# Performance work log

Hardware: AMD Instinct MI355X
Metric: run time of the kernel (lower is better)

Reference implementation:

```python
import jax, jax.numpy as jnp
import numpy as np

B, S, D, MD = 4, 4096, 1024, 512
SCALE = 0.02  # init scale for weights


def _layernorm(x, g, b, eps=1e-5):
    m = jnp.mean(x, axis=-1, keepdims=True)
    v = jnp.mean((x - m) ** 2, axis=-1, keepdims=True)
    return (x - m) * jax.lax.rsqrt(v + eps) * g + b


def _mem_mlp(h, W0, W1):
    # MemoryMLP depth=2: linear -> gelu -> linear (no biases)
    return jax.nn.gelu(h @ W0) @ W1


def _assoc_scan(gates, inputs):
    # state_t = g_t * state_{t-1} + in_t, over the seq axis (axis=1)
    def step(state, gi):
        g, i = gi
        s = g * state + i
        return s, s
    init = jnp.zeros_like(inputs[:, 0])
    _, out = jax.lax.scan(step, init, (jnp.moveaxis(gates, 1, 0), jnp.moveaxis(inputs, 1, 0)))
    return jnp.moveaxis(out, 1, 0)


def setup_inputs() -> dict:
    key = jax.random.key(0)
    ks = jax.random.split(key, 10)
    return {
        "x": jax.random.normal(ks[0], (B, S, D), jnp.float32),
        "Wd": jax.random.normal(ks[1], (D, MD), jnp.float32) * SCALE,
        "bd": jnp.zeros((MD,), jnp.float32),
        "Wu": jax.random.normal(ks[2], (MD, D), jnp.float32) * SCALE,
        "bu": jnp.zeros((D,), jnp.float32),
        "Wq": jax.random.normal(ks[3], (MD, MD), jnp.float32) * SCALE,
        "bq": jnp.zeros((MD,), jnp.float32),
        "Wk": jax.random.normal(ks[4], (MD, MD), jnp.float32) * SCALE,
        "bk": jnp.zeros((MD,), jnp.float32),
        "Wv": jax.random.normal(ks[5], (MD, MD), jnp.float32) * SCALE,
        "bv": jnp.zeros((MD,), jnp.float32),
        "q_gamma": jnp.ones((MD,), jnp.float32),
        "q_beta": jnp.zeros((MD,), jnp.float32),
        "k_gamma": jnp.ones((MD,), jnp.float32),
        "k_beta": jnp.zeros((MD,), jnp.float32),
        "W0": jax.random.normal(ks[6], (MD, MD), jnp.float32) * SCALE,
        "W1": jax.random.normal(ks[7], (MD, MD), jnp.float32) * SCALE,
        "adaptive_lr": jnp.full((1,), 0.01, jnp.float32),
        "forget_factor": jnp.full((1,), 0.1, jnp.float32),
    }


def reference(x, Wd, bd, Wu, bu, Wq, bq, Wk, bk, Wv, bv,
              q_gamma, q_beta, k_gamma, k_beta, W0, W1,
              adaptive_lr, forget_factor):
    h = x @ Wd + bd                                   # [B,S,MD] down_proj
    q = _layernorm(h @ Wq + bq, q_gamma, q_beta)      # q_norm(to_queries)
    k = _layernorm(h @ Wk + bk, k_gamma, k_beta)      # k_norm(to_keys)
    v = h @ Wv + bv                                   # to_values
    retrieved = _mem_mlp(q, W0, W1)                   # memory read
    pred = _mem_mlp(k, W0, W1)                        # memory store pred
    # per-token surprise: MSE over feature dim
    surprise = jnp.mean((pred - v) ** 2, axis=-1, keepdims=True)  # [B,S,1]
    gate_val = 1.0 - jax.nn.sigmoid(forget_factor)[0]
    gates = jnp.full((B, S, 1), 1.0, jnp.float32) * gate_val
    inputs = adaptive_lr[0] * surprise * v            # surprise-weighted write
    scanned = _assoc_scan(gates, inputs)              # sequential recurrence
    out = (retrieved + scanned) @ Wu + bu             # up_proj
    return out
```

## Files before the change

kernel.cpp:

```cpp
#include <hip/hip_runtime.h>
#include <hip/hip_bf16.h>
#include <math.h>

#define B_    4
#define S_    4096
#define DD    1024
#define MD    512
#define NTOK  16384
#define CHUNK 32
#define NCH   128

typedef unsigned short u16;
typedef unsigned int u32;
typedef __attribute__((ext_vector_type(8))) short short8;
typedef __attribute__((ext_vector_type(4))) float f32x4;
typedef __attribute__((ext_vector_type(4))) unsigned short us4;

__device__ __forceinline__ float bf2f(u16 u) {
    u32 x = ((u32)u) << 16;
    return __builtin_bit_cast(float, x);
}
__device__ __forceinline__ u16 f2bf(float f) {
    u32 x = __builtin_bit_cast(u32, f);
    u32 lsb = (x >> 16) & 1u;
    x += 0x7fffu + lsb;
    return (u16)(x >> 16);
}
__device__ __forceinline__ float gelu_f(float x) {
    float x3 = x * x * x;
    return 0.5f * x * (1.0f + tanhf(0.7978845608028654f * (x + 0.044715f * x3)));
}
__device__ __forceinline__ float gate_from_ff(const float* ff) {
    return 1.0f - 1.0f / (1.0f + expf(-ff[0]));
}

#define GLDS(gp, lp) __builtin_amdgcn_global_load_lds( \
    (const __attribute__((address_space(1))) void*)(gp), \
    (__attribute__((address_space(3))) void*)(lp), 16, 0, 0)

template<int EPI, int HB, int OUTBF>
__global__ __launch_bounds__(512) void gemm_bf16_k(
    const u16* __restrict__ A0, const u16* __restrict__ A1, const u16* __restrict__ A2,
    const u16* __restrict__ W0p, const u16* __restrict__ W1p, const u16* __restrict__ W2p,
    const float* __restrict__ c0, const float* __restrict__ c1, const float* __restrict__ c2,
    void* __restrict__ o0, void* __restrict__ o1, void* __restrict__ o2,
    int K, int OM)
{
    __shared__ __align__(16) u16 Al[3][256 * 32];
    __shared__ __align__(16) u16 Bl[3][128 * 32];
    const int tid = threadIdx.x;
    const int w = tid >> 6, l = tid & 63;

    const int z = blockIdx.z;
    const u16* A      = (z == 0) ? A0 : (z == 1) ? A1 : A2;
    const u16* BT     = (z == 0) ? W0p : (z == 1) ? W1p : W2p;
    const float* bias = (z == 0) ? c0 : (z == 1) ? c1 : c2;
    void* outp        = (z == 0) ? o0 : (z == 1) ? o1 : o2;

    const int rowBase = blockIdx.y * 256, colBase = blockIdx.x * 128;
    const int wm = (w >> 1) * 64, wn = (w & 1) * 64;
    const int lr = l & 15;

    float bj[4] = {0.f, 0.f, 0.f, 0.f};
    if (HB) {
#pragma unroll
        for (int n = 0; n < 4; ++n) bj[n] = bias[colBase + wn + n * 16 + lr];
        asm volatile("" :: "v"(bj[0]), "v"(bj[1]), "v"(bj[2]), "v"(bj[3]));
    }
    asm volatile("s_waitcnt vmcnt(0)" ::: "memory");
    __builtin_amdgcn_sched_barrier(0);

    const int srow = l >> 2;
    const int skoff = ((l & 3) ^ (srow & 3)) * 8;
    const u16* Ag0 = A  + (size_t)(rowBase + (2 * w) * 16 + srow) * K + skoff;
    const u16* Ag1 = A  + (size_t)(rowBase + (2 * w + 1) * 16 + srow) * K + skoff;
    const u16* Bg0 = BT + (size_t)(colBase + w * 16 + srow) * K + skoff;

    f32x4 acc[4][4];
#pragma unroll
    for (int i = 0; i < 4; ++i)
#pragma unroll
        for (int j = 0; j < 4; ++j) acc[i][j] = (f32x4){0.f, 0.f, 0.f, 0.f};

    const int KT = K >> 5;

#define STAGE(kt, buf) do { \
    const size_t ko = (size_t)(kt) << 5; \
    GLDS(Ag0 + ko, &Al[buf][((2 * w) * 16) * 32]); \
    GLDS(Ag1 + ko, &Al[buf][((2 * w + 1) * 16) * 32]); \
    GLDS(Bg0 + ko, &Bl[buf][(w * 16) * 32]); \
} while (0)

    STAGE(0, 0);
    STAGE(1, 1);
    asm volatile("s_waitcnt vmcnt(3)" ::: "memory");
    __builtin_amdgcn_sched_barrier(0);
    __builtin_amdgcn_s_barrier();
    __builtin_amdgcn_sched_barrier(0);

    const int rsw = (((l >> 4) ^ (l & 3)) << 3);
    int bt = 0;
    for (int t = 0; t < KT; ++t) {
        int bs = bt + 2; if (bs >= 3) bs -= 3;
        const bool more = (t + 2) < KT;
        if (more) STAGE(t + 2, bs);
        short8 af[4], bfr[4];
#pragma unroll
        for (int m = 0; m < 4; ++m)
            af[m] = *(const short8*)&Al[bt][(wm + m * 16 + lr) * 32 + rsw];
#pragma unroll
        for (int n = 0; n < 4; ++n)
            bfr[n] = *(const short8*)&Bl[bt][(wn + n * 16 + lr) * 32 + rsw];
#pragma unroll
        for (int m = 0; m < 4; ++m)
#pragma unroll
            for (int n = 0; n < 4; ++n)
                acc[m][n] = __builtin_amdgcn_mfma_f32_16x16x32_bf16(af[m], bfr[n], acc[m][n], 0, 0, 0);
        if (more) { asm volatile("s_waitcnt vmcnt(3)" ::: "memory"); }
        else      { asm volatile("s_waitcnt vmcnt(0)" ::: "memory"); }
        __builtin_amdgcn_sched_barrier(0);
        __builtin_amdgcn_s_barrier();
        __builtin_amdgcn_sched_barrier(0);
        bt = (bt + 1 == 3) ? 0 : bt + 1;
    }
#undef STAGE

    const int g4 = (l >> 4) * 4;
    const int col0 = colBase + wn;

    if (OUTBF) {
        u16* scr = &Al[0][0] + w * 1024;
        u16* ob = (u16*)outp;
        const bool odd = l & 1;
        const int lrp = lr & ~1;
#pragma unroll
        for (int m = 0; m < 4; ++m) {
            const int baseRow = rowBase + wm + m * 16;
            float vq[4][4];
#pragma unroll
            for (int n = 0; n < 4; ++n) {
#pragma unroll
                for (int q = 0; q < 4; ++q) {
                    float vv = acc[m][n][q] + bj[n];
                    if (EPI == 1) vv = gelu_f(vv);
                    vq[n][q] = vv;
                }
            }
#pragma unroll
            for (int n = 0; n < 4; ++n) {
                float pv[4];
#pragma unroll
                for (int q = 0; q < 4; ++q) pv[q] = __shfl_xor(vq[n][q], 1);
                const int q0 = odd ? 2 : 0;
#pragma unroll
                for (int j = 0; j < 2; ++j) {
                    const int qq = q0 + j;
                    float lo = odd ? pv[qq] : vq[n][qq];
                    float hi = odd ? vq[n][qq] : pv[qq];
                    u32 word = (u32)f2bf(lo) | ((u32)f2bf(hi) << 16);
                    *(u32*)&scr[(g4 + qq) * 64 + n * 16 + lrp] = word;
                }
            }
            asm volatile("s_waitcnt lgkmcnt(0)" ::: "memory");
            __builtin_amdgcn_sched_barrier(0);
            short8 r0 = *(const short8*)&scr[(l >> 3) * 64 + (l & 7) * 8];
            short8 r1 = *(const short8*)&scr[((l >> 3) + 8) * 64 + (l & 7) * 8];
            const size_t gaddr = (size_t)(baseRow + (l >> 3)) * OM + col0 + (l & 7) * 8;
            *(short8*)(ob + gaddr) = r0;
            *(short8*)(ob + gaddr + (size_t)8 * OM) = r1;
            __builtin_amdgcn_sched_barrier(0);
        }
    } else {
#pragma unroll
        for (int n = 0; n < 4; ++n) {
            const int col = col0 + n * 16 + lr;
#pragma unroll
            for (int m = 0; m < 4; ++m) {
                const int row0 = rowBase + wm + m * 16 + g4;
#pragma unroll
                for (int q = 0; q < 4; ++q) {
                    float vv = acc[m][n][q] + bj[n];
                    if (EPI == 1) vv = gelu_f(vv);
                    ((float*)outp)[(size_t)(row0 + q) * OM + col] = vv;
                }
            }
        }
    }
}

__global__ __launch_bounds__(256) void cvt_bf16_k(const float* __restrict__ in,
                                                  u16* __restrict__ out, int n)
{
    size_t i = ((size_t)blockIdx.x * 256 + threadIdx.x) * 8;
    if (i + 8 > (size_t)n) return;
    float4 a = *(const float4*)(in + i);
    float4 b = *(const float4*)(in + i + 4);
    short8 o;
    o[0] = (short)f2bf(a.x); o[1] = (short)f2bf(a.y);
    o[2] = (short)f2bf(a.z); o[3] = (short)f2bf(a.w);
    o[4] = (short)f2bf(b.x); o[5] = (short)f2bf(b.y);
    o[6] = (short)f2bf(b.z); o[7] = (short)f2bf(b.w);
    *(short8*)(out + i) = o;
}

__global__ __launch_bounds__(256) void wtrans_k(const float* __restrict__ W,
                                                u16* __restrict__ WT, int K, int M)
{
    __shared__ float t[32][33];
    const int tx = threadIdx.x, ty = threadIdx.y;
    const int m0 = blockIdx.x * 32, k0 = blockIdx.y * 32;
#pragma unroll
    for (int i = 0; i < 4; ++i)
        t[ty + i * 8][tx] = W[(size_t)(k0 + ty + i * 8) * M + m0 + tx];
    __syncthreads();
#pragma unroll
    for (int i = 0; i < 4; ++i)
        WT[(size_t)(m0 + ty + i * 8) * K + k0 + tx] = f2bf(t[tx][ty + i * 8]);
}

__global__ __launch_bounds__(256) void wtrans5_k(
    const float* __restrict__ Wa, const float* __restrict__ Wb,
    const float* __restrict__ Wc, const float* __restrict__ Wd_,
    const float* __restrict__ We,
    u16* __restrict__ Ta, u16* __restrict__ Tb, u16* __restrict__ Tc,
    u16* __restrict__ Td, u16* __restrict__ Te)
{
    __shared__ float t[32][33];
    const float* W; u16* T;
    switch (blockIdx.z) {
        case 0: W = Wa; T = Ta; break;
        case 1: W = Wb; T = Tb; break;
        case 2: W = Wc; T = Tc; break;
        case 3: W = Wd_; T = Td; break;
        default: W = We; T = Te; break;
    }
    const int tx = threadIdx.x, ty = threadIdx.y;
    const int m0 = blockIdx.x * 32, k0 = blockIdx.y * 32;
#pragma unroll
    for (int i = 0; i < 4; ++i)
        t[ty + i * 8][tx] = W[(size_t)(k0 + ty + i * 8) * 512 + m0 + tx];
    __syncthreads();
#pragma unroll
    for (int i = 0; i < 4; ++i)
        T[(size_t)(m0 + ty + i * 8) * 512 + k0 + tx] = f2bf(t[tx][ty + i * 8]);
}

__global__ __launch_bounds__(256) void ln2_k(u16* __restrict__ X0, u16* __restrict__ X1,
                                             const float* __restrict__ g0, const float* __restrict__ b0,
                                             const float* __restrict__ g1, const float* __restrict__ b1)
{
    const int row = blockIdx.x, tid = threadIdx.x;
    u16* x = (blockIdx.y ? X1 : X0) + (size_t)row * MD;
    const float* g = blockIdx.y ? g1 : g0;
    const float* b = blockIdx.y ? b1 : b0;
    float v0 = bf2f(x[tid]), v1 = bf2f(x[tid + 256]);
    float s = v0 + v1, q = v0 * v0 + v1 * v1;
#pragma unroll
    for (int off = 32; off > 0; off >>= 1) {
        s += __shfl_down(s, off);
        q += __shfl_down(q, off);
    }
    __shared__ float redS[4], redQ[4];
    __shared__ float s_mean, s_rstd;
    const int lane = tid & 63, w = tid >> 6;
    if (lane == 0) { redS[w] = s; redQ[w] = q; }
    __syncthreads();
    if (tid == 0) {
        float S = redS[0] + redS[1] + redS[2] + redS[3];
        float Q = redQ[0] + redQ[1] + redQ[2] + redQ[3];
        float m = S * (1.f / 512.f);
        float var = Q * (1.f / 512.f) - m * m;
        s_mean = m; s_rstd = rsqrtf(var + 1e-5f);
    }
    __syncthreads();
    const float m = s_mean, rs = s_rstd;
    x[tid]       = f2bf((v0 - m) * rs * g[tid]       + b[tid]);
    x[tid + 256] = f2bf((v1 - m) * rs * g[tid + 256] + b[tid + 256]);
}

__global__ __launch_bounds__(256) void surprise_k(const u16* __restrict__ pred,
                                                  const u16* __restrict__ v,
                                                  const float* __restrict__ lr_p,
                                                  float* __restrict__ coef)
{
    const int row = blockIdx.x, tid = threadIdx.x;
    const u16* pp = pred + (size_t)row * MD;
    const u16* vp = v + (size_t)row * MD;
    float d0 = bf2f(pp[tid]) - bf2f(vp[tid]);
    float d1 = bf2f(pp[tid + 256]) - bf2f(vp[tid + 256]);
    float q = d0 * d0 + d1 * d1;
#pragma unroll
    for (int off = 32; off > 0; off >>= 1) q += __shfl_down(q, off);
    __shared__ float redQ[4];
    const int lane = tid & 63, w = tid >> 6;
    if (lane == 0) redQ[w] = q;
    __syncthreads();
    if (tid == 0) {
        float Q = redQ[0] + redQ[1] + redQ[2] + redQ[3];
        coef[row] = lr_p[0] * (Q * (1.f / 512.f));
    }
}

__global__ __launch_bounds__(256) void scan1_k(u16* __restrict__ io,
                                               const float* __restrict__ coef,
                                               const float* __restrict__ ff,
                                               float* __restrict__ carry)
{
    const int idx = blockIdx.x * blockDim.x + threadIdx.x;
    const int d4 = (idx & 127) * 4;
    const int c = (idx >> 7) & (NCH - 1);
    const int b = idx >> 14;
    const float g = gate_from_ff(ff);
    const int tok0 = b * S_ + c * CHUNK;
    u16* p = io + (size_t)tok0 * MD + d4;
    const float* cf = coef + tok0;
    float s0 = 0.f, s1 = 0.f, s2 = 0.f, s3 = 0.f;
#pragma unroll 4
    for (int t = 0; t < CHUNK; ++t) {
        us4 vv = *(const us4*)(p + (size_t)t * MD);
        const float ct = cf[t];
        s0 = fmaf(g, s0, ct * bf2f(vv.x));
        s1 = fmaf(g, s1, ct * bf2f(vv.y));
        s2 = fmaf(g, s2, ct * bf2f(vv.z));
        s3 = fmaf(g, s3, ct * bf2f(vv.w));
        us4 ov = { f2bf(s0), f2bf(s1), f2bf(s2), f2bf(s3) };
        *(us4*)(p + (size_t)t * MD) = ov;
    }
    float4 cw = { s0, s1, s2, s3 };
    *(float4*)(carry + ((size_t)b * NCH + c) * MD + d4) = cw;
}

__global__ __launch_bounds__(256) void scan2_k(const float* __restrict__ carry,
                                               const float* __restrict__ ff,
                                               float* __restrict__ Sin)
{
    const int idx = blockIdx.x * blockDim.x + threadIdx.x;
    const int d = idx & (MD - 1);
    const int b = idx >> 9;
    const float g = gate_from_ff(ff);
    const float gL = powf(g, (float)CHUNK);
    float p = 0.f;
    for (int c = 0; c < NCH; ++c) {
        Sin[((size_t)b * NCH + c) * MD + d] = p;
        p = carry[((size_t)b * NCH + c) * MD + d] + gL * p;
    }
}

__global__ __launch_bounds__(256) void scan3_k(const u16* __restrict__ loc,
                                               const float* __restrict__ Sin,
                                               const u16* __restrict__ retr,
                                               const float* __restrict__ ff,
                                               u16* __restrict__ fin)
{
    const size_t idx = (size_t)blockIdx.x * blockDim.x + threadIdx.x;
    const int d4 = (int)(idx & 127) * 4;
    const int t = (int)((idx >> 7) & (S_ - 1));
    const int b = (int)(idx >> 19);
    const int c = t >> 5, tl = t & (CHUNK - 1);
    const float g = gate_from_ff(ff);
    const float f = exp2f((float)(tl + 1) * log2f(g));
    const size_t row = (size_t)(b * S_ + t) * MD + d4;
    us4 lv = *(const us4*)(loc + row);
    us4 rv = *(const us4*)(retr + row);
    float4 sv = *(const float4*)(Sin + ((size_t)b * NCH + c) * MD + d4);
    us4 ov;
    ov.x = f2bf(bf2f(lv.x) + f * sv.x + bf2f(rv.x));
    ov.y = f2bf(bf2f(lv.y) + f * sv.y + bf2f(rv.y));
    ov.z = f2bf(bf2f(lv.z) + f * sv.z + bf2f(rv.z));
    ov.w = f2bf(bf2f(lv.w) + f * sv.w + bf2f(rv.w));
    *(us4*)(fin + row) = ov;
}

extern "C" void kernel_launch(void* const* d_in, const int* in_sizes, int n_in,
                              void* d_out, int out_size, void* d_ws, size_t ws_size,
                              hipStream_t stream) {
    const float* x   = (const float*)d_in[0];
    const float* Wd  = (const float*)d_in[1];
    const float* bd  = (const float*)d_in[2];
    const float* Wu  = (const float*)d_in[3];
    const float* bu  = (const float*)d_in[4];
    const float* Wq  = (const float*)d_in[5];
    const float* bq  = (const float*)d_in[6];
    const float* Wk  = (const float*)d_in[7];
    const float* bk  = (const float*)d_in[8];
    const float* Wv  = (const float*)d_in[9];
    const float* bv  = (const float*)d_in[10];
    const float* qg  = (const float*)d_in[11];
    const float* qb  = (const float*)d_in[12];
    const float* kg  = (const float*)d_in[13];
    const float* kb  = (const float*)d_in[14];
    const float* W0  = (const float*)d_in[15];
    const float* W1  = (const float*)d_in[16];
    const float* lr  = (const float*)d_in[17];
    const float* ff  = (const float*)d_in[18];
    float* out = (float*)d_out;

    u16* wdT   = (u16*)d_ws;
    u16* wqT   = wdT + 512 * 1024;
    u16* wkT   = wqT + 512 * 512;
    u16* wvT   = wkT + 512 * 512;
    u16* w0T   = wvT + 512 * 512;
    u16* w1T   = w0T + 512 * 512;
    u16* wuT   = w1T + 512 * 512;
    u16* xb    = wuT + 1024 * 512;
    u16* hb    = xb + (size_t)NTOK * DD;
    u16* b1    = hb + (size_t)NTOK * MD;
    u16* b2    = b1 + (size_t)NTOK * MD;
    u16* VB    = b2 + (size_t)NTOK * MD;
    float* coef  = (float*)(VB + (size_t)NTOK * MD);
    float* carry = coef + NTOK;
    float* Sin   = carry + (size_t)B_ * NCH * MD;
    u16* ax0 = xb;
    u16* ax1 = xb + (size_t)NTOK * MD;

    dim3 blk(256);
    dim3 gblk(512);
    dim3 t32(32, 8);

    cvt_bf16_k<<<(NTOK * DD) / (256 * 8), blk, 0, stream>>>(x, xb, NTOK * DD);
    wtrans_k<<<dim3(16, 32), t32, 0, stream>>>(Wd, wdT, 1024, 512);
    wtrans5_k<<<dim3(16, 16, 5), t32, 0, stream>>>(Wq, Wk, Wv, W0, W1,
        wqT, wkT, wvT, w0T, w1T);
    wtrans_k<<<dim3(32, 16), t32, 0, stream>>>(Wu, wuT, 512, 1024);

    gemm_bf16_k<0, 1, 1><<<dim3(4, 64, 1), gblk, 0, stream>>>(
        xb, xb, xb, wdT, wdT, wdT, bd, bd, bd, hb, hb, hb, 1024, 512);
    gemm_bf16_k<0, 1, 1><<<dim3(4, 64, 3), gblk, 0, stream>>>(
        hb, hb, hb, wqT, wkT, wvT, bq, bk, bv, b1, b2, VB, 512, 512);
    ln2_k<<<dim3(NTOK, 2), blk, 0, stream>>>(b1, b2, qg, qb, kg, kb);
    gemm_bf16_k<1, 0, 1><<<dim3(4, 64, 2), gblk, 0, stream>>>(
        b1, b2, b2, w0T, w0T, w0T, nullptr, nullptr, nullptr, ax0, ax1, ax1, 512, 512);
    gemm_bf16_k<0, 0, 1><<<dim3(4, 64, 2), gblk, 0, stream>>>(
        ax0, ax1, ax1, w1T, w1T, w1T, nullptr, nullptr, nullptr, b1, b2, b2, 512, 512);
    surprise_k<<<NTOK, blk, 0, stream>>>(b2, VB, lr, coef);
    scan1_k<<<(B_ * NCH * (MD / 4)) / 256, blk, 0, stream>>>(VB, coef, ff, carry);
    scan2_k<<<(B_ * MD) / 256, blk, 0, stream>>>(carry, ff, Sin);
    scan3_k<<<(NTOK * (MD / 4)) / 256, blk, 0, stream>>>(VB, Sin, b1, ff, hb);
    gemm_bf16_k<0, 1, 0><<<dim3(8, 64, 1), gblk, 0, stream>>>(
        hb, hb, hb, wuT, wuT, wuT, bu, bu, bu, out, out, out, 512, 1024);
}
```

Before: 341.4 us.

## Replace LDS-pipelined GEMM with direct-global-load MFMA GEMM and XCD-aware tile mapping

Replaces the 512-thread GEMM, which staged A/B tiles into LDS through a triple-buffered global_load_lds pipeline with barriers, with a 256-thread kernel that loads MFMA fragments straight from global memory into registers. Tiles shrink to 128x128, K becomes a compile-time constant, and a 1D grid is remapped so consecutive blocks on each XCD share row panels for L2 reuse. It removes LDS traffic and barriers but depends on cache hits for fragment reuse, and the per-lane 16-byte loads are strided with no explicit prefetch, so memory latency may be exposed.

New measurement: 535.9 us. +57.0%, slower.

```diff
diff --git a/kernel.cpp b/kernel.cpp
--- a/kernel.cpp
+++ b/kernel.cpp
@@ -34,102 +34,70 @@
     return 1.0f - 1.0f / (1.0f + expf(-ff[0]));
 }
 
-#define GLDS(gp, lp) __builtin_amdgcn_global_load_lds( \
-    (const __attribute__((address_space(1))) void*)(gp), \
-    (__attribute__((address_space(3))) void*)(lp), 16, 0, 0)
-
-template<int EPI, int HB, int OUTBF>
-__global__ __launch_bounds__(512) void gemm_bf16_k(
+template<int KT, int LCB, int EPI, int HB, int OUTBF>
+__global__ __launch_bounds__(256) void sgemm_k(
     const u16* __restrict__ A0, const u16* __restrict__ A1, const u16* __restrict__ A2,
-    const u16* __restrict__ W0p, const u16* __restrict__ W1p, const u16* __restrict__ W2p,
+    const u16* __restrict__ B0, const u16* __restrict__ B1, const u16* __restrict__ B2,
     const float* __restrict__ c0, const float* __restrict__ c1, const float* __restrict__ c2,
     void* __restrict__ o0, void* __restrict__ o1, void* __restrict__ o2,
-    int K, int OM)
-{
-    __shared__ __align__(16) u16 Al[3][256 * 32];
-    __shared__ __align__(16) u16 Bl[3][128 * 32];
+    int OM)
+{
+    constexpr int K = KT * 32;
+    __shared__ __align__(16) u16 scr_s[4096];
     const int tid = threadIdx.x;
     const int w = tid >> 6, l = tid & 63;
 
     const int z = blockIdx.z;
     const u16* A      = (z == 0) ? A0 : (z == 1) ? A1 : A2;
-    const u16* BT     = (z == 0) ? W0p : (z == 1) ? W1p : W2p;
+    const u16* BT     = (z == 0) ? B0 : (z == 1) ? B1 : B2;
     const float* bias = (z == 0) ? c0 : (z == 1) ? c1 : c2;
     void* outp        = (z == 0) ? o0 : (z == 1) ? o1 : o2;
 
-    const int rowBase = blockIdx.y * 256, colBase = blockIdx.x * 128;
+    const int bid = blockIdx.x;
+    const int xcd = bid & 7, j = bid >> 3;
+    const int panel = xcd * 16 + (j >> LCB);
+    const int colb  = j & ((1 << LCB) - 1);
+    const int rowBase = panel * 128, colBase = colb * 128;
     const int wm = (w >> 1) * 64, wn = (w & 1) * 64;
     const int lr = l & 15;
-
+    const int ko = (l >> 4) * 8;
+
+    const u16* Ap = A  + (size_t)(rowBase + wm + lr) * K + ko;
+    const u16* Bp = BT + (size_t)(colBase + wn + lr) * K + ko;
+
+    f32x4 acc[4][4];
+#pragma unroll
+    for (int i = 0; i < 4; ++i)
+#pragma unroll
+        for (int jj = 0; jj < 4; ++jj) acc[i][jj] = (f32x4){0.f, 0.f, 0.f, 0.f};
+
+#pragma unroll 2
+    for (int kt = 0; kt < KT; ++kt) {
+        const int kb = kt * 32;
+        short8 af[4], bfr[4];
+#pragma unroll
+        for (int m = 0; m < 4; ++m)
+            af[m] = *(const short8*)(Ap + (size_t)m * 16 * K + kb);
+#pragma unroll
+        for (int n = 0; n < 4; ++n)
+            bfr[n] = *(const short8*)(Bp + (size_t)n * 16 * K + kb);
+#pragma unroll
+        for (int m = 0; m < 4; ++m)
+#pragma unroll
+            for (int n = 0; n < 4; ++n)
+                acc[m][n] = __builtin_amdgcn_mfma_f32_16x16x32_bf16(af[m], bfr[n], acc[m][n], 0, 0, 0);
+    }
+
+    const int g4 = (l >> 4) * 4;
+    const int col0 = colBase + wn;
     float bj[4] = {0.f, 0.f, 0.f, 0.f};
     if (HB) {
 #pragma unroll
-        for (int n = 0; n < 4; ++n) bj[n] = bias[colBase + wn + n * 16 + lr];
-        asm volatile("" :: "v"(bj[0]), "v"(bj[1]), "v"(bj[2]), "v"(bj[3]));
-    }
-    asm volatile("s_waitcnt vmcnt(0)" ::: "memory");
-    __builtin_amdgcn_sched_barrier(0);
-
-    const int srow = l >> 2;
-    const int skoff = ((l & 3) ^ (srow & 3)) * 8;
-    const u16* Ag0 = A  + (size_t)(rowBase + (2 * w) * 16 + srow) * K + skoff;
-    const u16* Ag1 = A  + (size_t)(rowBase + (2 * w + 1) * 16 + srow) * K + skoff;
-    const u16* Bg0 = BT + (size_t)(colBase + w * 16 + srow) * K + skoff;
-
-    f32x4 acc[4][4];
-#pragma unroll
-    for (int i = 0; i < 4; ++i)
-#pragma unroll
-        for (int j = 0; j < 4; ++j) acc[i][j] = (f32x4){0.f, 0.f, 0.f, 0.f};
-
-    const int KT = K >> 5;
-
-#define STAGE(kt, buf) do { \
-    const size_t ko = (size_t)(kt) << 5; \
-    GLDS(Ag0 + ko, &Al[buf][((2 * w) * 16) * 32]); \
-    GLDS(Ag1 + ko, &Al[buf][((2 * w + 1) * 16) * 32]); \
-    GLDS(Bg0 + ko, &Bl[buf][(w * 16) * 32]); \
-} while (0)
-
-    STAGE(0, 0);
-    STAGE(1, 1);
-    asm volatile("s_waitcnt vmcnt(3)" ::: "memory");
-    __builtin_amdgcn_sched_barrier(0);
-    __builtin_amdgcn_s_barrier();
-    __builtin_amdgcn_sched_barrier(0);
-
-    const int rsw = (((l >> 4) ^ (l & 3)) << 3);
-    int bt = 0;
-    for (int t = 0; t < KT; ++t) {
-        int bs = bt + 2; if (bs >= 3) bs -= 3;
-        const bool more = (t + 2) < KT;
-        if (more) STAGE(t + 2, bs);
-        short8 af[4], bfr[4];
-#pragma unroll
-        for (int m = 0; m < 4; ++m)
-            af[m] = *(const short8*)&Al[bt][(wm + m * 16 + lr) * 32 + rsw];
-#pragma unroll
-        for (int n = 0; n < 4; ++n)
-            bfr[n] = *(const short8*)&Bl[bt][(wn + n * 16 + lr) * 32 + rsw];
-#pragma unroll
-        for (int m = 0; m < 4; ++m)
-#pragma unroll
-            for (int n = 0; n < 4; ++n)
-                acc[m][n] = __builtin_amdgcn_mfma_f32_16x16x32_bf16(af[m], bfr[n], acc[m][n], 0, 0, 0);
-        if (more) { asm volatile("s_waitcnt vmcnt(3)" ::: "memory"); }
-        else      { asm volatile("s_waitcnt vmcnt(0)" ::: "memory"); }
-        __builtin_amdgcn_sched_barrier(0);
-        __builtin_amdgcn_s_barrier();
-        __builtin_amdgcn_sched_barrier(0);
-        bt = (bt + 1 == 3) ? 0 : bt + 1;
-    }
-#undef STAGE
-
-    const int g4 = (l >> 4) * 4;
-    const int col0 = colBase + wn;
+        for (int n = 0; n < 4; ++n) bj[n] = bias[col0 + n * 16 + lr];
+    }
 
     if (OUTBF) {
-        u16* scr = &Al[0][0] + w * 1024;
+        u16* scr = scr_s + w * 1024;
         u16* ob = (u16*)outp;
         const bool odd = l & 1;
         const int lrp = lr & ~1;
@@ -153,8 +121,8 @@
                 for (int q = 0; q < 4; ++q) pv[q] = __shfl_xor(vq[n][q], 1);
                 const int q0 = odd ? 2 : 0;
 #pragma unroll
-                for (int j = 0; j < 2; ++j) {
-                    const int qq = q0 + j;
+                for (int jj = 0; jj < 2; ++jj) {
+                    const int qq = q0 + jj;
                     float lo = odd ? pv[qq] : vq[n][qq];
                     float hi = odd ? vq[n][qq] : pv[qq];
                     u32 word = (u32)f2bf(lo) | ((u32)f2bf(hi) << 16);
@@ -414,7 +382,6 @@
     u16* ax1 = xb + (size_t)NTOK * MD;
 
     dim3 blk(256);
-    dim3 gblk(512);
     dim3 t32(32, 8);
 
     cvt_bf16_k<<<(NTOK * DD) / (256 * 8), blk, 0, stream>>>(x, xb, NTOK * DD);
@@ -423,19 +390,19 @@
         wqT, wkT, wvT, w0T, w1T);
     wtrans_k<<<dim3(32, 16), t32, 0, stream>>>(Wu, wuT, 512, 1024);
 
-    gemm_bf16_k<0, 1, 1><<<dim3(4, 64, 1), gblk, 0, stream>>>(
-        xb, xb, xb, wdT, wdT, wdT, bd, bd, bd, hb, hb, hb, 1024, 512);
-    gemm_bf16_k<0, 1, 1><<<dim3(4, 64, 3), gblk, 0, stream>>>(
-        hb, hb, hb, wqT, wkT, wvT, bq, bk, bv, b1, b2, VB, 512, 512);
+    sgemm_k<32, 2, 0, 1, 1><<<dim3(512, 1, 1), blk, 0, stream>>>(
+        xb, xb, xb, wdT, wdT, wdT, bd, bd, bd, hb, hb, hb, 512);
+    sgemm_k<16, 2, 0, 1, 1><<<dim3(512, 1, 3), blk, 0, stream>>>(
+        hb, hb, hb, wqT, wkT, wvT, bq, bk, bv, b1, b2, VB, 512);
     ln2_k<<<dim3(NTOK, 2), blk, 0, stream>>>(b1, b2, qg, qb, kg, kb);
-    gemm_bf16_k<1, 0, 1><<<dim3(4, 64, 2), gblk, 0, stream>>>(
-        b1, b2, b2, w0T, w0T, w0T, nullptr, nullptr, nullptr, ax0, ax1, ax1, 512, 512);
-    gemm_bf16_k<0, 0, 1><<<dim3(4, 64, 2), gblk, 0, stream>>>(
-        ax0, ax1, ax1, w1T, w1T, w1T, nullptr, nullptr, nullptr, b1, b2, b2, 512, 512);
+    sgemm_k<16, 2, 1, 0, 1><<<dim3(512, 1, 2), blk, 0, stream>>>(
+        b1, b2, b2, w0T, w0T, w0T, nullptr, nullptr, nullptr, ax0, ax1, ax1, 512);
+    sgemm_k<16, 2, 0, 0, 1><<<dim3(512, 1, 2), blk, 0, stream>>>(
+        ax0, ax1, ax1, w1T, w1T, w1T, nullptr, nullptr, nullptr, b1, b2, b2, 512);
     surprise_k<<<NTOK, blk, 0, stream>>>(b2, VB, lr, coef);
     scan1_k<<<(B_ * NCH * (MD / 4)) / 256, blk, 0, stream>>>(VB, coef, ff, carry);
     scan2_k<<<(B_ * MD) / 256, blk, 0, stream>>>(carry, ff, Sin);
     scan3_k<<<(NTOK * (MD / 4)) / 256, blk, 0, stream>>>(VB, Sin, b1, ff, hb);
-    gemm_bf16_k<0, 1, 0><<<dim3(8, 64, 1), gblk, 0, stream>>>(
-        hb, hb, hb, wuT, wuT, wuT, bu, bu, bu, out, out, out, 512, 1024);
-}
+    sgemm_k<16, 3, 0, 1, 0><<<dim3(1024, 1, 1), blk, 0, stream>>>(
+        hb, hb, hb, wuT, wuT, wuT, bu, bu, bu, out, out, out, 1024);
+}
```
